# Kernel optimization log

Hardware: AMD Instinct MI355X
Metric: run time of the kernel (lower is better)

Reference implementation:

```python
import jax, jax.numpy as jnp
import numpy as np

B, T, E, U, V = 512, 256, 256, 512, 10000


def _lstm_scan(x_seq, Wx, Wh, b, reverse=False):
    # x_seq: [B, T, E]; returns final (h, c), each [B, U]
    def step(carry, x_t):
        h, c = carry
        gates = x_t @ Wx + h @ Wh + b  # [B, 4U]
        i, f, g, o = jnp.split(gates, 4, axis=-1)
        i = jax.nn.sigmoid(i)
        f = jax.nn.sigmoid(f)
        o = jax.nn.sigmoid(o)
        g = jnp.tanh(g)
        c = f * c + i * g
        h = o * jnp.tanh(c)
        return (h, c), None

    init = (jnp.zeros((x_seq.shape[0], U), x_seq.dtype),
            jnp.zeros((x_seq.shape[0], U), x_seq.dtype))
    xs = jnp.swapaxes(x_seq, 0, 1)  # [T, B, E]
    (h, c), _ = jax.lax.scan(step, init, xs, reverse=reverse)
    return h, c


def setup_inputs() -> dict:
    key = jax.random.key(0)
    ks = jax.random.split(key, 12)
    s = lambda k, shape, scale: jax.random.normal(k, shape, jnp.float32) * scale
    return {
        "sentence": jax.random.randint(ks[0], (B, T), 0, V),
        "emb": s(ks[1], (V, E), 0.05),
        "Wx_fw": s(ks[2], (E, 4 * U), 1.0 / np.sqrt(E)),
        "Wh_fw": s(ks[3], (U, 4 * U), 1.0 / np.sqrt(U)),
        "b_fw": jnp.zeros((4 * U,), jnp.float32),
        "Wx_bw": s(ks[4], (E, 4 * U), 1.0 / np.sqrt(E)),
        "Wh_bw": s(ks[5], (U, 4 * U), 1.0 / np.sqrt(U)),
        "b_bw": jnp.zeros((4 * U,), jnp.float32),
        "W1": s(ks[6], (2 * U, 64), 1.0 / np.sqrt(2 * U)),
        "b1": jnp.zeros((64,), jnp.float32),
        "W2": s(ks[7], (64, V), 1.0 / np.sqrt(64)),
        "b2": jnp.zeros((V,), jnp.float32),
    }


def reference(sentence, emb, Wx_fw, Wh_fw, b_fw, Wx_bw, Wh_bw, b_bw, W1, b1, W2, b2):
    x = emb[sentence]  # [B, T, E]
    h_fw, _ = _lstm_scan(x, Wx_fw, Wh_fw, b_fw, reverse=False)
    # backward loop iterates t = T-1 .. 0, i.e. consumes the sequence reversed
    h_bw, _ = _lstm_scan(x, Wx_bw, Wh_bw, b_bw, reverse=True)
    h = jnp.concatenate([h_fw, h_bw], axis=-1)  # [B, 2U]
    hidden = jax.nn.relu(h @ W1 + b1)
    return jax.nn.softmax(hidden @ W2 + b2, axis=-1)
```

## Files before the change

kernel.cpp:

```cpp
#include <hip/hip_runtime.h>

#define Bb 512
#define Tt 256
#define Ee 256
#define Uu 512
#define Vv 10000

#define PACKB_OFF 0
#define HBUF_OFF  6291456
#define HID_OFF   8388608
#define CNT_OFF   8519680
#define EMB_OFF   12582912

typedef __attribute__((ext_vector_type(8))) short short8;
typedef __attribute__((ext_vector_type(4))) float f32x4;

__device__ __forceinline__ float bf2f(ushort u) {
  union { unsigned int i; float f; } v; v.i = ((unsigned int)u) << 16; return v.f;
}
__device__ __forceinline__ ushort f2bf(float f) {
  union { float f; unsigned int i; } v; v.f = f;
  unsigned int x = v.i;
  return (ushort)((x + 0x7fffu + ((x >> 16) & 1u)) >> 16);
}
__device__ __forceinline__ float fast_sigmoid(float x) {
  return 1.f / (1.f + __expf(-x));
}
__device__ __forceinline__ float fast_tanh(float x) {
  float t = __expf(-2.f * fabsf(x));
  float r = (1.f - t) / (1.f + t);
  return x >= 0.f ? r : -r;
}

__device__ __forceinline__ short8 load_h16(const ushort* p) {
  union { unsigned long long u[2]; short8 s; } v;
  v.u[0] = __hip_atomic_load((const unsigned long long*)p,     __ATOMIC_RELAXED, __HIP_MEMORY_SCOPE_AGENT);
  v.u[1] = __hip_atomic_load((const unsigned long long*)p + 1, __ATOMIC_RELAXED, __HIP_MEMORY_SCOPE_AGENT);
  return v.s;
}
__device__ __forceinline__ void store_h(ushort* p, ushort v) {
  __hip_atomic_store(p, v, __ATOMIC_RELAXED, __HIP_MEMORY_SCOPE_AGENT);
}

__global__ __launch_bounds__(256) void init_zero(char* ob)
{
  if (blockIdx.x < 512) {
    uint4 z; z.x = 0; z.y = 0; z.z = 0; z.w = 0;
    ((uint4*)(ob + HBUF_OFF))[(size_t)blockIdx.x * 256 + threadIdx.x] = z;
  } else {
    ((unsigned int*)(ob + CNT_OFF))[threadIdx.x] = 0u;
  }
}

__global__ __launch_bounds__(256) void conv_emb(const float* __restrict__ emb, char* ob)
{
  ushort* embB = (ushort*)(ob + EMB_OFF);
  size_t i = ((size_t)blockIdx.x * 256 + threadIdx.x) * 8;
  f32x4 f0 = *(const f32x4*)(emb + i);
  f32x4 f1 = *(const f32x4*)(emb + i + 4);
  short8 v;
  #pragma unroll
  for (int j = 0; j < 4; j++) {
    v[j]     = (short)f2bf(f0[j]);
    v[4 + j] = (short)f2bf(f1[j]);
  }
  *(short8*)(embB + i) = v;
}

__global__ __launch_bounds__(256) void pack_weights(
    const float* __restrict__ Wx_fw, const float* __restrict__ Wh_fw,
    const float* __restrict__ Wx_bw, const float* __restrict__ Wh_bw,
    char* ob)
{
  __shared__ ushort tile[32][520];
  ushort* packB = (ushort*)(ob + PACKB_OFF);
  const int cq = blockIdx.x;
  const int ks = blockIdx.y;
  const int d  = blockIdx.z;
  const int tid = threadIdx.x;
  const float* Wx = d ? Wx_bw : Wx_fw;
  const float* Wh = d ? Wh_bw : Wh_fw;
  const int colbase = cq * 512;

  #pragma unroll
  for (int i = 0; i < 8; i++) {
    int chunk = tid + i * 256;
    int row = chunk >> 6;
    int cc = (chunk & 63) * 8;
    int k = ks * 32 + row;
    const float* src = (k < Ee) ? (Wx + (size_t)k * 2048 + colbase + cc)
                                : (Wh + (size_t)(k - Ee) * 2048 + colbase + cc);
    f32x4 f0 = *(const f32x4*)src;
    f32x4 f1 = *(const f32x4*)(src + 4);
    #pragma unroll
    for (int j = 0; j < 4; j++) {
      tile[row][cc + j]     = f2bf(f0[j]);
      tile[row][cc + 4 + j] = f2bf(f1[j]);
    }
  }
  __syncthreads();
  #pragma unroll
  for (int i = 0; i < 8; i++) {
    int chunk = tid + i * 256;
    int ctl = chunk >> 6;
    int lane = chunk & 63;
    int quad = lane >> 4, l15 = lane & 15;
    short8 v;
    #pragma unroll
    for (int jj = 0; jj < 8; jj++)
      v[jj] = (short)tile[quad * 8 + jj][ctl * 16 + l15];
    int ct = (colbase >> 4) + ctl;
    *(short8*)(packB + (((size_t)(d * 128 + ct) * 24 + ks) * 512) + lane * 8) = v;
  }
}

__global__ __launch_bounds__(256) void lstm_persistent(
    char* ob, const int* __restrict__ sent,
    const float* __restrict__ b_fw, const float* __restrict__ b_bw)
{
  __shared__ ushort ldsB[32768];
  const ushort* packB = (const ushort*)(ob + PACKB_OFF);
  const ushort* embB  = (const ushort*)(ob + EMB_OFF);
  ushort* hbuf = (ushort*)(ob + HBUF_OFF);

  const int utp = blockIdx.x;
  const int bt  = blockIdx.y;
  const int d   = blockIdx.z;
  unsigned int* cnt = (unsigned int*)(ob + CNT_OFF) + (d * 4 + bt) * 32;

  const int tid = threadIdx.x;
  const int w = tid >> 6, lane = tid & 63;
  const int l15 = lane & 15, quad = lane >> 4;
  const int mbase = bt * 128 + w * 32;
  const int u = utp * 16 + l15;

  for (int i = 0; i < 16; i++) {
    int c = tid + i * 256;
    int lc = c & 63, qc = (c >> 6) & 3, k8 = c >> 8;
    const ushort* src = packB +
        ((size_t)(d * 128 + qc * 32 + utp) * 24 + 8 + k8) * 512 + lc * 8;
    *(short8*)&ldsB[(k8 * 4 + qc) * 512 + lc * 8] = *(const short8*)src;
  }

  const float* bias = d ? b_bw : b_fw;
  const float bi  = bias[u];
  const float bfv = bias[512 + u];
  const float bg  = bias[1024 + u];
  const float bo  = bias[1536 + u];

  const ushort* bembP[4];
  #pragma unroll
  for (int q = 0; q < 4; q++)
    bembP[q] = packB + ((size_t)(d * 128 + q * 32 + utp) * 24) * 512 + lane * 8;

  float creg[2][4];
  #pragma unroll
  for (int a = 0; a < 2; a++)
    #pragma unroll
    for (int r = 0; r < 4; r++) creg[a][r] = 0.f;

  __syncthreads();

  for (int s = 0; s < Tt; s++) {
    const int t = d ? (Tt - 1 - s) : s;
    const ushort* hread  = hbuf + (size_t)((s & 1) * 2 + d) * Bb * Uu;
    ushort*       hwrite = hbuf + (size_t)((((s & 1) ^ 1) * 2) + d) * Bb * Uu;

    f32x4 acc[2][4];
    #pragma unroll
    for (int a = 0; a < 2; a++)
      #pragma unroll
      for (int q = 0; q < 4; q++)
        acc[a][q] = (f32x4){0.f, 0.f, 0.f, 0.f};

    const int tok0 = sent[(mbase + l15) * Tt + t];
    const int tok1 = sent[(mbase + 16 + l15) * Tt + t];
    const ushort* e0 = embB + (size_t)tok0 * Ee + quad * 8;
    const ushort* e1 = embB + (size_t)tok1 * Ee + quad * 8;

    #pragma unroll
    for (int ks = 0; ks < 8; ks++) {
      short8 bq0 = *(const short8*)(bembP[0] + ks * 512);
      short8 bq1 = *(const short8*)(bembP[1] + ks * 512);
      short8 bq2 = *(const short8*)(bembP[2] + ks * 512);
      short8 bq3 = *(const short8*)(bembP[3] + ks * 512);
      short8 a0 = *(const short8*)(e0 + ks * 32);
      short8 a1 = *(const short8*)(e1 + ks * 32);
      acc[0][0] = __builtin_amdgcn_mfma_f32_16x16x32_bf16(a0, bq0, acc[0][0], 0, 0, 0);
      acc[0][1] = __builtin_amdgcn_mfma_f32_16x16x32_bf16(a0, bq1, acc[0][1], 0, 0, 0);
      acc[0][2] = __builtin_amdgcn_mfma_f32_16x16x32_bf16(a0, bq2, acc[0][2], 0, 0, 0);
      acc[0][3] = __builtin_amdgcn_mfma_f32_16x16x32_bf16(a0, bq3, acc[0][3], 0, 0, 0);
      acc[1][0] = __builtin_amdgcn_mfma_f32_16x16x32_bf16(a1, bq0, acc[1][0], 0, 0, 0);
      acc[1][1] = __builtin_amdgcn_mfma_f32_16x16x32_bf16(a1, bq1, acc[1][1], 0, 0, 0);
      acc[1][2] = __builtin_amdgcn_mfma_f32_16x16x32_bf16(a1, bq2, acc[1][2], 0, 0, 0);
      acc[1][3] = __builtin_amdgcn_mfma_f32_16x16x32_bf16(a1, bq3, acc[1][3], 0, 0, 0);
    }

    if (tid == 0) {
      const unsigned int target = 32u * (unsigned int)s;
      while (__hip_atomic_fetch_add(cnt, 0u, __ATOMIC_RELAXED,
                                    __HIP_MEMORY_SCOPE_AGENT) < target)
        __builtin_amdgcn_s_sleep(2);
    }
    __syncthreads();

    const ushort* h0 = hread + (size_t)(mbase + l15) * Uu + quad * 8;
    const ushort* h1 = hread + (size_t)(mbase + 16 + l15) * Uu + quad * 8;
    #pragma unroll
    for (int k8 = 0; k8 < 16; k8++) {
      short8 bq0 = *(const short8*)&ldsB[(k8 * 4 + 0) * 512 + lane * 8];
      short8 bq1 = *(const short8*)&ldsB[(k8 * 4 + 1) * 512 + lane * 8];
      short8 bq2 = *(const short8*)&ldsB[(k8 * 4 + 2) * 512 + lane * 8];
      short8 bq3 = *(const short8*)&ldsB[(k8 * 4 + 3) * 512 + lane * 8];
      short8 a0 = load_h16(h0 + k8 * 32);
      short8 a1 = load_h16(h1 + k8 * 32);
      acc[0][0] = __builtin_amdgcn_mfma_f32_16x16x32_bf16(a0, bq0, acc[0][0], 0, 0, 0);
      acc[0][1] = __builtin_amdgcn_mfma_f32_16x16x32_bf16(a0, bq1, acc[0][1], 0, 0, 0);
      acc[0][2] = __builtin_amdgcn_mfma_f32_16x16x32_bf16(a0, bq2, acc[0][2], 0, 0, 0);
      acc[0][3] = __builtin_amdgcn_mfma_f32_16x16x32_bf16(a0, bq3, acc[0][3], 0, 0, 0);
      acc[1][0] = __builtin_amdgcn_mfma_f32_16x16x32_bf16(a1, bq0, acc[1][0], 0, 0, 0);
      acc[1][1] = __builtin_amdgcn_mfma_f32_16x16x32_bf16(a1, bq1, acc[1][1], 0, 0, 0);
      acc[1][2] = __builtin_amdgcn_mfma_f32_16x16x32_bf16(a1, bq2, acc[1][2], 0, 0, 0);
      acc[1][3] = __builtin_amdgcn_mfma_f32_16x16x32_bf16(a1, bq3, acc[1][3], 0, 0, 0);
    }

    #pragma unroll
    for (int a = 0; a < 2; a++) {
      #pragma unroll
      for (int r = 0; r < 4; r++) {
        float iv = fast_sigmoid(acc[a][0][r] + bi);
        float fv = fast_sigmoid(acc[a][1][r] + bfv);
        float gv = fast_tanh(acc[a][2][r] + bg);
        float ov = fast_sigmoid(acc[a][3][r] + bo);
        float cn = fv * creg[a][r] + iv * gv;
        creg[a][r] = cn;
        int m = mbase + a * 16 + quad * 4 + r;
        store_h(hwrite + (size_t)m * Uu + u, f2bf(ov * fast_tanh(cn)));
      }
    }

    __syncthreads();
    if (tid == 0)
      __hip_atomic_fetch_add(cnt, 1u, __ATOMIC_RELAXED, __HIP_MEMORY_SCOPE_AGENT);
  }
}

__global__ __launch_bounds__(256) void hidden_kernel(
    char* ob, const float* __restrict__ W1, const float* __restrict__ b1)
{
  const ushort* hbuf = (const ushort*)(ob + HBUF_OFF);
  float* hidden = (float*)(ob + HID_OFF);
  int m = blockIdx.x * 4 + (threadIdx.x >> 6);
  int col = threadIdx.x & 63;
  const ushort* hf = hbuf + (size_t)m * Uu;
  const ushort* hb = hbuf + (size_t)(Bb + m) * Uu;
  float acc = b1[col];
  for (int k = 0; k < 512; k++) acc += bf2f(hf[k]) * W1[k * 64 + col];
  for (int k = 0; k < 512; k++) acc += bf2f(hb[k]) * W1[(512 + k) * 64 + col];
  hidden[(size_t)m * 64 + col] = fmaxf(acc, 0.f);
}

__device__ __forceinline__ void softmax_row(
    const float* hs, const float* __restrict__ W2, const float* __restrict__ b2,
    float* out, int m, float* red)
{
  const int tid = threadIdx.x;
  float lg[40];
  float mx = -1e30f;
  #pragma unroll 4
  for (int i = 0; i < 40; i++) {
    int c = tid + i * 256;
    float a = -1e30f;
    if (c < Vv) {
      a = b2[c];
      for (int k = 0; k < 64; k++) a += hs[k] * W2[(size_t)k * Vv + c];
    }
    lg[i] = a;
    mx = fmaxf(mx, a);
  }
  red[tid] = mx; __syncthreads();
  for (int off = 128; off > 0; off >>= 1) {
    if (tid < off) red[tid] = fmaxf(red[tid], red[tid + off]);
    __syncthreads();
  }
  mx = red[0];
  __syncthreads();

  float sum = 0.f;
  #pragma unroll 4
  for (int i = 0; i < 40; i++) {
    int c = tid + i * 256;
    if (c < Vv) { lg[i] = __expf(lg[i] - mx); sum += lg[i]; }
  }
  red[tid] = sum; __syncthreads();
  for (int off = 128; off > 0; off >>= 1) {
    if (tid < off) red[tid] += red[tid + off];
    __syncthreads();
  }
  float inv = 1.f / red[0];
  __syncthreads();
  #pragma unroll 4
  for (int i = 0; i < 40; i++) {
    int c = tid + i * 256;
    if (c < Vv) out[(size_t)m * Vv + c] = lg[i] * inv;
  }
}

__global__ __launch_bounds__(256) void logits_main(
    char* ob, const float* __restrict__ W2, const float* __restrict__ b2)
{
  __shared__ float hs[64];
  __shared__ float red[256];
  const float* hidden = (const float*)(ob + HID_OFF);
  float* out = (float*)ob;
  int bx = blockIdx.x;
  int m = (bx < 209) ? bx : (bx + 4);
  if (threadIdx.x < 64) hs[threadIdx.x] = hidden[(size_t)m * 64 + threadIdx.x];
  __syncthreads();
  softmax_row(hs, W2, b2, out, m, red);
}

__global__ __launch_bounds__(256) void logits_tail(
    char* ob, const float* __restrict__ W2, const float* __restrict__ b2)
{
  __shared__ float hs4[4][64];
  __shared__ float red[256];
  const float* hidden = (const float*)(ob + HID_OFF);
  float* out = (float*)ob;
  {
    int r = threadIdx.x >> 6, col = threadIdx.x & 63;
    hs4[r][col] = hidden[(size_t)(209 + r) * 64 + col];
  }
  __syncthreads();
  for (int r = 0; r < 4; r++) {
    softmax_row(hs4[r], W2, b2, out, 209 + r, red);
    __syncthreads();
  }
}

extern "C" void kernel_launch(void* const* d_in, const int* in_sizes, int n_in,
                              void* d_out, int out_size, void* d_ws, size_t ws_size,
                              hipStream_t stream)
{
  const int*   sent  = (const int*)d_in[0];
  const float* emb   = (const float*)d_in[1];
  const float* Wx_fw = (const float*)d_in[2];
  const float* Wh_fw = (const float*)d_in[3];
  const float* b_fw  = (const float*)d_in[4];
  const float* Wx_bw = (const float*)d_in[5];
  const float* Wh_bw = (const float*)d_in[6];
  const float* b_bw  = (const float*)d_in[7];
  const float* W1    = (const float*)d_in[8];
  const float* b1    = (const float*)d_in[9];
  const float* W2    = (const float*)d_in[10];
  const float* b2    = (const float*)d_in[11];
  char* ob = (char*)d_out;
  (void)d_ws; (void)ws_size; (void)in_sizes; (void)n_in; (void)out_size;

  init_zero<<<513, 256, 0, stream>>>(ob);
  pack_weights<<<dim3(4, 24, 2), 256, 0, stream>>>(Wx_fw, Wh_fw, Wx_bw, Wh_bw, ob);
  conv_emb<<<1250, 256, 0, stream>>>(emb, ob);

  lstm_persistent<<<dim3(32, 4, 2), 256, 0, stream>>>(ob, sent, b_fw, b_bw);

  hidden_kernel<<<128, 256, 0, stream>>>(ob, W1, b1);
  logits_main<<<508, 256, 0, stream>>>(ob, W2, b2);
  logits_tail<<<1,   256, 0, stream>>>(ob, W2, b2);
}
```

Before: 4.251 ms.

## Split LSTM batch across twice as many persistent blocks, pack h stores into 64-bit

The persistent LSTM grid doubles from 256 to 512 blocks, and each wave now handles 16 batch rows instead of 32, so each block covers 64 rows. This halves the serial MFMA and gate work per step and should use more CUs. The h output is packed with lane shuffles so that one lane writes four bf16 values as a single 64-bit atomic store, replacing four scalar 16-bit stores. The spin-wait now uses an atomic load instead of fetch_add, with a shorter sleep. The trade-off is more blocks synchronizing on each counter and re-reading the packed weights from LDS.

```diff
diff --git a/kernel.cpp b/kernel.cpp
--- a/kernel.cpp
+++ b/kernel.cpp
@@ -38,9 +38,6 @@
   v.u[1] = __hip_atomic_load((const unsigned long long*)p + 1, __ATOMIC_RELAXED, __HIP_MEMORY_SCOPE_AGENT);
   return v.s;
 }
-__device__ __forceinline__ void store_h(ushort* p, ushort v) {
-  __hip_atomic_store(p, v, __ATOMIC_RELAXED, __HIP_MEMORY_SCOPE_AGENT);
-}
 
 __global__ __launch_bounds__(256) void init_zero(char* ob)
 {
@@ -48,7 +45,8 @@
     uint4 z; z.x = 0; z.y = 0; z.z = 0; z.w = 0;
     ((uint4*)(ob + HBUF_OFF))[(size_t)blockIdx.x * 256 + threadIdx.x] = z;
   } else {
-    ((unsigned int*)(ob + CNT_OFF))[threadIdx.x] = 0u;
+    uint2 z2; z2.x = 0; z2.y = 0;
+    ((uint2*)(ob + CNT_OFF))[threadIdx.x] = z2;
   }
 }
 
@@ -126,12 +124,13 @@
   const int utp = blockIdx.x;
   const int bt  = blockIdx.y;
   const int d   = blockIdx.z;
-  unsigned int* cnt = (unsigned int*)(ob + CNT_OFF) + (d * 4 + bt) * 32;
+  unsigned int* cnt = (unsigned int*)(ob + CNT_OFF) + (d * 8 + bt) * 32;
 
   const int tid = threadIdx.x;
   const int w = tid >> 6, lane = tid & 63;
   const int l15 = lane & 15, quad = lane >> 4;
-  const int mbase = bt * 128 + w * 32;
+  const int mbase = bt * 64;
+  const int mrow0 = mbase + w * 16;
   const int u = utp * 16 + l15;
 
   for (int i = 0; i < 16; i++) {
@@ -153,11 +152,9 @@
   for (int q = 0; q < 4; q++)
     bembP[q] = packB + ((size_t)(d * 128 + q * 32 + utp) * 24) * 512 + lane * 8;
 
-  float creg[2][4];
-  #pragma unroll
-  for (int a = 0; a < 2; a++)
-    #pragma unroll
-    for (int r = 0; r < 4; r++) creg[a][r] = 0.f;
+  float creg[4];
+  #pragma unroll
+  for (int r = 0; r < 4; r++) creg[r] = 0.f;
 
   __syncthreads();
 
@@ -166,76 +163,66 @@
     const ushort* hread  = hbuf + (size_t)((s & 1) * 2 + d) * Bb * Uu;
     ushort*       hwrite = hbuf + (size_t)((((s & 1) ^ 1) * 2) + d) * Bb * Uu;
 
-    f32x4 acc[2][4];
-    #pragma unroll
-    for (int a = 0; a < 2; a++)
-      #pragma unroll
-      for (int q = 0; q < 4; q++)
-        acc[a][q] = (f32x4){0.f, 0.f, 0.f, 0.f};
-
-    const int tok0 = sent[(mbase + l15) * Tt + t];
-    const int tok1 = sent[(mbase + 16 + l15) * Tt + t];
-    const ushort* e0 = embB + (size_t)tok0 * Ee + quad * 8;
-    const ushort* e1 = embB + (size_t)tok1 * Ee + quad * 8;
+    f32x4 acc[4];
+    #pragma unroll
+    for (int q = 0; q < 4; q++) acc[q] = (f32x4){0.f, 0.f, 0.f, 0.f};
+
+    const int tok = sent[(mrow0 + l15) * Tt + t];
+    const ushort* e0 = embB + (size_t)tok * Ee + quad * 8;
 
     #pragma unroll
     for (int ks = 0; ks < 8; ks++) {
+      short8 a0 = *(const short8*)(e0 + ks * 32);
       short8 bq0 = *(const short8*)(bembP[0] + ks * 512);
       short8 bq1 = *(const short8*)(bembP[1] + ks * 512);
       short8 bq2 = *(const short8*)(bembP[2] + ks * 512);
       short8 bq3 = *(const short8*)(bembP[3] + ks * 512);
-      short8 a0 = *(const short8*)(e0 + ks * 32);
-      short8 a1 = *(const short8*)(e1 + ks * 32);
-      acc[0][0] = __builtin_amdgcn_mfma_f32_16x16x32_bf16(a0, bq0, acc[0][0], 0, 0, 0);
-      acc[0][1] = __builtin_amdgcn_mfma_f32_16x16x32_bf16(a0, bq1, acc[0][1], 0, 0, 0);
-      acc[0][2] = __builtin_amdgcn_mfma_f32_16x16x32_bf16(a0, bq2, acc[0][2], 0, 0, 0);
-      acc[0][3] = __builtin_amdgcn_mfma_f32_16x16x32_bf16(a0, bq3, acc[0][3], 0, 0, 0);
-      acc[1][0] = __builtin_amdgcn_mfma_f32_16x16x32_bf16(a1, bq0, acc[1][0], 0, 0, 0);
-      acc[1][1] = __builtin_amdgcn_mfma_f32_16x16x32_bf16(a1, bq1, acc[1][1], 0, 0, 0);
-      acc[1][2] = __builtin_amdgcn_mfma_f32_16x16x32_bf16(a1, bq2, acc[1][2], 0, 0, 0);
-      acc[1][3] = __builtin_amdgcn_mfma_f32_16x16x32_bf16(a1, bq3, acc[1][3], 0, 0, 0);
+      acc[0] = __builtin_amdgcn_mfma_f32_16x16x32_bf16(a0, bq0, acc[0], 0, 0, 0);
+      acc[1] = __builtin_amdgcn_mfma_f32_16x16x32_bf16(a0, bq1, acc[1], 0, 0, 0);
+      acc[2] = __builtin_amdgcn_mfma_f32_16x16x32_bf16(a0, bq2, acc[2], 0, 0, 0);
+      acc[3] = __builtin_amdgcn_mfma_f32_16x16x32_bf16(a0, bq3, acc[3], 0, 0, 0);
     }
 
     if (tid == 0) {
       const unsigned int target = 32u * (unsigned int)s;
-      while (__hip_atomic_fetch_add(cnt, 0u, __ATOMIC_RELAXED,
-                                    __HIP_MEMORY_SCOPE_AGENT) < target)
-        __builtin_amdgcn_s_sleep(2);
-    }
-    __syncthreads();
-
-    const ushort* h0 = hread + (size_t)(mbase + l15) * Uu + quad * 8;
-    const ushort* h1 = hread + (size_t)(mbase + 16 + l15) * Uu + quad * 8;
+      while (__hip_atomic_load(cnt, __ATOMIC_RELAXED,
+                               __HIP_MEMORY_SCOPE_AGENT) < target)
+        __builtin_amdgcn_s_sleep(1);
+    }
+    __syncthreads();
+
+    const ushort* h0 = hread + (size_t)(mrow0 + l15) * Uu + quad * 8;
     #pragma unroll
     for (int k8 = 0; k8 < 16; k8++) {
+      short8 a0 = load_h16(h0 + k8 * 32);
       short8 bq0 = *(const short8*)&ldsB[(k8 * 4 + 0) * 512 + lane * 8];
       short8 bq1 = *(const short8*)&ldsB[(k8 * 4 + 1) * 512 + lane * 8];
       short8 bq2 = *(const short8*)&ldsB[(k8 * 4 + 2) * 512 + lane * 8];
       short8 bq3 = *(const short8*)&ldsB[(k8 * 4 + 3) * 512 + lane * 8];
-      short8 a0 = load_h16(h0 + k8 * 32);
-      short8 a1 = load_h16(h1 + k8 * 32);
-      acc[0][0] = __builtin_amdgcn_mfma_f32_16x16x32_bf16(a0, bq0, acc[0][0], 0, 0, 0);
-      acc[0][1] = __builtin_amdgcn_mfma_f32_16x16x32_bf16(a0, bq1, acc[0][1], 0, 0, 0);
-      acc[0][2] = __builtin_amdgcn_mfma_f32_16x16x32_bf16(a0, bq2, acc[0][2], 0, 0, 0);
-      acc[0][3] = __builtin_amdgcn_mfma_f32_16x16x32_bf16(a0, bq3, acc[0][3], 0, 0, 0);
-      acc[1][0] = __builtin_amdgcn_mfma_f32_16x16x32_bf16(a1, bq0, acc[1][0], 0, 0, 0);
-      acc[1][1] = __builtin_amdgcn_mfma_f32_16x16x32_bf16(a1, bq1, acc[1][1], 0, 0, 0);
-      acc[1][2] = __builtin_amdgcn_mfma_f32_16x16x32_bf16(a1, bq2, acc[1][2], 0, 0, 0);
-      acc[1][3] = __builtin_amdgcn_mfma_f32_16x16x32_bf16(a1, bq3, acc[1][3], 0, 0, 0);
-    }
-
-    #pragma unroll
-    for (int a = 0; a < 2; a++) {
-      #pragma unroll
-      for (int r = 0; r < 4; r++) {
-        float iv = fast_sigmoid(acc[a][0][r] + bi);
-        float fv = fast_sigmoid(acc[a][1][r] + bfv);
-        float gv = fast_tanh(acc[a][2][r] + bg);
-        float ov = fast_sigmoid(acc[a][3][r] + bo);
-        float cn = fv * creg[a][r] + iv * gv;
-        creg[a][r] = cn;
-        int m = mbase + a * 16 + quad * 4 + r;
-        store_h(hwrite + (size_t)m * Uu + u, f2bf(ov * fast_tanh(cn)));
+      acc[0] = __builtin_amdgcn_mfma_f32_16x16x32_bf16(a0, bq0, acc[0], 0, 0, 0);
+      acc[1] = __builtin_amdgcn_mfma_f32_16x16x32_bf16(a0, bq1, acc[1], 0, 0, 0);
+      acc[2] = __builtin_amdgcn_mfma_f32_16x16x32_bf16(a0, bq2, acc[2], 0, 0, 0);
+      acc[3] = __builtin_amdgcn_mfma_f32_16x16x32_bf16(a0, bq3, acc[3], 0, 0, 0);
+    }
+
+    #pragma unroll
+    for (int r = 0; r < 4; r++) {
+      float iv = fast_sigmoid(acc[0][r] + bi);
+      float fv = fast_sigmoid(acc[1][r] + bfv);
+      float gv = fast_tanh(acc[2][r] + bg);
+      float ov = fast_sigmoid(acc[3][r] + bo);
+      float cn = fv * creg[r] + iv * gv;
+      creg[r] = cn;
+      unsigned int x = f2bf(ov * fast_tanh(cn));
+      unsigned int y = (unsigned int)__shfl_xor((int)x, 1);
+      unsigned int w01 = x | (y << 16);
+      unsigned int w23 = (unsigned int)__shfl_xor((int)w01, 2);
+      if ((l15 & 3) == 0) {
+        int m = mrow0 + quad * 4 + r;
+        unsigned long long v8 = ((unsigned long long)w23 << 32) | w01;
+        __hip_atomic_store(
+            (unsigned long long*)(hwrite + (size_t)m * Uu + utp * 16 + l15),
+            v8, __ATOMIC_RELAXED, __HIP_MEMORY_SCOPE_AGENT);
       }
     }
 
@@ -361,7 +348,7 @@
   pack_weights<<<dim3(4, 24, 2), 256, 0, stream>>>(Wx_fw, Wh_fw, Wx_bw, Wh_bw, ob);
   conv_emb<<<1250, 256, 0, stream>>>(emb, ob);
 
-  lstm_persistent<<<dim3(32, 4, 2), 256, 0, stream>>>(ob, sent, b_fw, b_bw);
+  lstm_persistent<<<dim3(32, 8, 2), 256, 0, stream>>>(ob, sent, b_fw, b_bw);
 
   hidden_kernel<<<128, 256, 0, stream>>>(ob, W1, b1);
   logits_main<<<508, 256, 0, stream>>>(ob, W2, b2);
```

New measurement: 4.188 ms. About the same (-1.5%).
